# Performance work log

Measured on AMD Instinct MI355X. Metric: run time of the kernel, lower is better.

The kernel has to match this reference:

```python
import jax, jax.numpy as jnp
import numpy as np

L = 2048      # seq_len
E = 2048      # hidden_dim
H = 16        # num_heads
D = E // H    # head_dim


def setup_inputs() -> dict:
    key = jax.random.key(0)
    ks = jax.random.split(key, 6)
    x = jax.random.normal(ks[0], (L, E), dtype=jnp.float32)
    bias_matrix = jax.random.normal(ks[1], (L, L), dtype=jnp.float32) * 0.1
    # nn.MultiheadAttention params: packed in_proj [3E, E] + bias [3E], out_proj [E, E] + bias [E]
    in_proj_weight = jax.random.normal(ks[2], (3 * E, E), dtype=jnp.float32) * 0.02
    in_proj_bias = jax.random.normal(ks[3], (3 * E,), dtype=jnp.float32) * 0.02
    out_proj_weight = jax.random.normal(ks[4], (E, E), dtype=jnp.float32) * 0.02
    out_proj_bias = jax.random.normal(ks[5], (E,), dtype=jnp.float32) * 0.02
    return {
        "x": x,
        "bias_matrix": bias_matrix,
        "in_proj_weight": in_proj_weight,
        "in_proj_bias": in_proj_bias,
        "out_proj_weight": out_proj_weight,
        "out_proj_bias": out_proj_bias,
    }


def reference(x, bias_matrix, in_proj_weight, in_proj_bias, out_proj_weight, out_proj_bias):
    # Packed QKV projection (torch Linear convention: y = x @ W.T + b)
    qkv = x @ in_proj_weight.T + in_proj_bias            # [L, 3E]
    q, k, v = jnp.split(qkv, 3, axis=-1)                 # each [L, E]
    q = q.reshape(L, H, D)
    k = k.reshape(L, H, D)
    v = v.reshape(L, H, D)
    scale = 1.0 / jnp.sqrt(jnp.asarray(D, dtype=x.dtype))
    # scores: [H, L, L]; bias_matrix broadcast over heads (torch 2D attn_mask semantics)
    scores = jnp.einsum("lhd,mhd->hlm", q * scale, k) + bias_matrix[None, :, :]
    attn = jax.nn.softmax(scores, axis=-1)
    ctx = jnp.einsum("hlm,mhd->lhd", attn, v).reshape(L, E)
    out = ctx @ out_proj_weight.T + out_proj_bias        # [L, E]
    return out
```

## Files before the change

### kernel.cpp

```cpp
#include <hip/hip_runtime.h>
#include <math.h>

#define L_SEQ 2048
#define E_DIM 2048
#define H_NUM 16
#define D_HEAD 128

typedef __attribute__((ext_vector_type(8))) _Float16 half8;
typedef __attribute__((ext_vector_type(4))) _Float16 half4;
typedef __attribute__((ext_vector_type(4))) float floatx4;

static __device__ __forceinline__ void gload16(const void* g, void* lds) {
  __builtin_amdgcn_global_load_lds(
      (const __attribute__((address_space(1))) void*)g,
      (__attribute__((address_space(3))) void*)lds, 16, 0, 0);
}

__global__ __launch_bounds__(256)
void cvt3_f32_f16(const float* __restrict__ a, _Float16* __restrict__ oa, int na,
                  const float* __restrict__ b, _Float16* __restrict__ ob, int nb,
                  const float* __restrict__ c, _Float16* __restrict__ oc, int nc) {
  int i = (blockIdx.x * 256 + threadIdx.x) * 8;
  const float* src;
  _Float16* dst;
  if (i < na) {
    src = a + i; dst = oa + i;
  } else if (i < na + nb) {
    src = b + (i - na); dst = ob + (i - na);
  } else if (i < na + nb + nc) {
    src = c + (i - na - nb); dst = oc + (i - na - nb);
  } else {
    return;
  }
  float4 p = *(const float4*)src;
  float4 q = *(const float4*)(src + 4);
  half8 h = {(_Float16)p.x, (_Float16)p.y, (_Float16)p.z, (_Float16)p.w,
             (_Float16)q.x, (_Float16)q.y, (_Float16)q.z, (_Float16)q.w};
  *(half8*)dst = h;
}

__global__ __launch_bounds__(512, 1)
void gemm_qkv(const _Float16* __restrict__ A, const _Float16* __restrict__ B,
              const float* __restrict__ bias, _Float16* __restrict__ qk,
              _Float16* __restrict__ vt) {
  constexpr int K = E_DIM;
  __shared__ __align__(16) char smem[131072];
  char* const Asm = smem;
  char* const Bsm = smem + 32768;

  const int tid = threadIdx.x;
  const int wave = tid >> 6, lane = tid & 63;
  const int l15 = lane & 15, quad = lane >> 4;
  const int wm = wave >> 2, wn = wave & 3;

  const int lid = blockIdx.y * 16 + blockIdx.x;
  const int swz = (lid & 7) * 32 + (lid >> 3);
  const int brow = (swz >> 4) * 128, bcol = (swz & 15) * 384;

  const _Float16* Ag = A + (size_t)brow * K;
  const _Float16* Bg = B + (size_t)bcol * K;

  auto stg = [&](int T, int kh) {
    char* aslot = Asm + ((T & 1) * 2 + kh) * 8192;
    char* bslot = Bsm + ((T & 1) * 2 + kh) * 24576;
    {
      int row = tid >> 2, c = tid & 3;
      gload16(Ag + (size_t)row * K + T * 64 + kh * 32 +
                  ((c ^ ((row >> 1) & 3)) * 8),
              aslot + (tid & ~63) * 16);
    }
#pragma unroll
    for (int j = 0; j < 3; ++j) {
      int mb = j * 512 + (tid & ~63);
      int m = mb + (tid & 63);
      int row = m >> 2, c = m & 3;
      gload16(Bg + (size_t)row * K + T * 64 + kh * 32 +
                  ((c ^ ((row >> 1) & 3)) * 8),
              bslot + mb * 16);
    }
  };

  floatx4 acc[4][6];
#pragma unroll
  for (int i = 0; i < 4; ++i)
#pragma unroll
    for (int j = 0; j < 6; ++j) acc[i][j] = (floatx4){0.f, 0.f, 0.f, 0.f};

  auto compute_phase = [&](int T, int ks) {
    const char* Ab = Asm + ((T & 1) * 2 + ks) * 8192;
    const char* Bb = Bsm + ((T & 1) * 2 + ks) * 24576;
    half8 af[4], bf[6];
#pragma unroll
    for (int t = 0; t < 4; ++t) {
      int r = wm * 64 + t * 16 + l15;
      af[t] = *(const half8*)(Ab + (size_t)r * 64 +
                              ((quad ^ ((r >> 1) & 3)) * 16));
    }
#pragma unroll
    for (int t = 0; t < 6; ++t) {
      int r = wn * 96 + t * 16 + l15;
      bf[t] = *(const half8*)(Bb + (size_t)r * 64 +
                              ((quad ^ ((r >> 1) & 3)) * 16));
    }
#pragma unroll
    for (int i = 0; i < 4; ++i)
#pragma unroll
      for (int j = 0; j < 6; ++j)
        acc[i][j] = __builtin_amdgcn_mfma_f32_16x16x32_f16(af[i], bf[j],
                                                           acc[i][j], 0, 0, 0);
  };

  stg(0, 0); stg(0, 1); stg(1, 0);

  for (int T = 0; T < 31; ++T) {
    __builtin_amdgcn_sched_barrier(0);
    asm volatile("s_waitcnt vmcnt(8) lgkmcnt(0)" ::: "memory");
    __builtin_amdgcn_s_barrier();
    __builtin_amdgcn_sched_barrier(0);
    stg(T + 1, 1);
    compute_phase(T, 0);
    __builtin_amdgcn_sched_barrier(0);
    asm volatile("s_waitcnt vmcnt(8) lgkmcnt(0)" ::: "memory");
    __builtin_amdgcn_s_barrier();
    __builtin_amdgcn_sched_barrier(0);
    if (T < 30) stg(T + 2, 0);
    compute_phase(T, 1);
  }
  __builtin_amdgcn_sched_barrier(0);
  asm volatile("s_waitcnt vmcnt(4) lgkmcnt(0)" ::: "memory");
  __builtin_amdgcn_s_barrier();
  __builtin_amdgcn_sched_barrier(0);
  compute_phase(31, 0);
  __builtin_amdgcn_sched_barrier(0);
  asm volatile("s_waitcnt vmcnt(0) lgkmcnt(0)" ::: "memory");
  __builtin_amdgcn_s_barrier();
  __builtin_amdgcn_sched_barrier(0);
  compute_phase(31, 1);

  const int crow = brow + wm * 64;
  const int ccol0 = bcol + wn * 96;
#pragma unroll
  for (int j = 0; j < 6; ++j) {
    int col = ccol0 + j * 16 + l15;
    float bb = bias[col];
    if (col < 2 * E_DIM) {
#pragma unroll
      for (int i = 0; i < 4; ++i)
#pragma unroll
        for (int r = 0; r < 4; ++r)
          qk[(size_t)(crow + i * 16 + quad * 4 + r) * (2 * E_DIM) + col] =
              (_Float16)(acc[i][j][r] + bb);
    } else {
      int vrow = col - 2 * E_DIM;
#pragma unroll
      for (int i = 0; i < 4; ++i) {
        int rbase = crow + i * 16 + quad * 4;
        half4 h = {(_Float16)(acc[i][j][0] + bb), (_Float16)(acc[i][j][1] + bb),
                   (_Float16)(acc[i][j][2] + bb), (_Float16)(acc[i][j][3] + bb)};
        *(half4*)&vt[(size_t)vrow * L_SEQ + rbase] = h;
      }
    }
  }
}

template <int TM, int TN, int WR, int WC>
__global__ __launch_bounds__(256)
void gemm_mfma(const _Float16* __restrict__ A, const _Float16* __restrict__ B,
               const float* __restrict__ bias, float* __restrict__ C,
               int M, int N, int K) {
  constexpr int RT = TM / (16 * WR);
  constexpr int CT = TN / (16 * WC);
  constexpr int ACH = TM / 8;
  constexpr int NCH = (TM + TN) / 32;

  __shared__ _Float16 As[2][TM * 64];
  __shared__ _Float16 Bs[2][TN * 64];

  const int tid = threadIdx.x;
  const int wave = tid >> 6, lane = tid & 63;
  const int l15 = lane & 15, quad = lane >> 4;
  const int wr = wave / WC, wc = wave % WC;
  const int row0 = blockIdx.y * TM, col0 = blockIdx.x * TN;

  const int srow = lane >> 3;
  const int gc = (lane & 7) ^ srow;

  auto stage = [&](int buf, int k0) {
#pragma unroll
    for (int c = 0; c < NCH; ++c) {
      int chunk = wave * NCH + c;
      if (chunk < ACH) {
        int row = chunk * 8 + srow;
        gload16((const char*)(A + (size_t)(row0 + row) * K + k0) + gc * 16,
                (char*)&As[buf][0] + chunk * 1024);
      } else {
        int bch = chunk - ACH;
        int row = bch * 8 + srow;
        gload16((const char*)(B + (size_t)(col0 + row) * K + k0) + gc * 16,
                (char*)&Bs[buf][0] + bch * 1024);
      }
    }
  };

  floatx4 acc[RT][CT];
#pragma unroll
  for (int i = 0; i < RT; ++i)
#pragma unroll
    for (int j = 0; j < CT; ++j) acc[i][j] = (floatx4){0.f, 0.f, 0.f, 0.f};

  const int niter = K / 64;
  stage(0, 0);

  for (int it = 0; it < niter; ++it) {
    const int cur = it & 1;
    __syncthreads();
    if (it + 1 < niter) stage(cur ^ 1, (it + 1) * 64);

#pragma unroll
    for (int ks = 0; ks < 2; ++ks) {
      half8 af[RT], bf[CT];
#pragma unroll
      for (int t = 0; t < RT; ++t) {
        int r = wr * (16 * RT) + t * 16 + l15;
        af[t] = *(const half8*)&As[cur][r * 64 + (((ks * 4 + quad) ^ (r & 7)) * 8)];
      }
#pragma unroll
      for (int t = 0; t < CT; ++t) {
        int r = wc * (16 * CT) + t * 16 + l15;
        bf[t] = *(const half8*)&Bs[cur][r * 64 + (((ks * 4 + quad) ^ (r & 7)) * 8)];
      }
#pragma unroll
      for (int tr = 0; tr < RT; ++tr)
#pragma unroll
        for (int tc = 0; tc < CT; ++tc)
          acc[tr][tc] = __builtin_amdgcn_mfma_f32_16x16x32_f16(
              af[tr], bf[tc], acc[tr][tc], 0, 0, 0);
    }
  }

  const int crow = row0 + wr * (16 * RT);
  const int ccol = col0 + wc * (16 * CT);

#pragma unroll
  for (int tc = 0; tc < CT; ++tc) {
    int col = ccol + tc * 16 + l15;
    float bb = bias[col];
#pragma unroll
    for (int tr = 0; tr < RT; ++tr)
#pragma unroll
      for (int r = 0; r < 4; ++r)
        C[(size_t)(crow + tr * 16 + quad * 4 + r) * N + col] =
            acc[tr][tc][r] + bb;
  }
}

__global__ __launch_bounds__(512, 2)
void attn_mfma(const _Float16* __restrict__ qk, const _Float16* __restrict__ vt,
               const float* __restrict__ bias, _Float16* __restrict__ ctx) {
  const int h = blockIdx.x;
  const int q0 = blockIdx.y * 128;
  const int tid = threadIdx.x;
  const int wave = tid >> 6;
  const int lane = tid & 63;
  const int l15 = lane & 15;
  const int quad = lane >> 4;

  __shared__ _Float16 Ks[2][64][136];
  __shared__ _Float16 Vst[2][128][72];
  __shared__ _Float16 Ps[128][72];

  half8 qa[4];
  {
    const _Float16* qp = qk + (size_t)(q0 + wave * 16 + l15) * (2 * E_DIM) +
                         h * D_HEAD + quad * 8;
#pragma unroll
    for (int ks = 0; ks < 4; ++ks) qa[ks] = *(const half8*)(qp + ks * 32);
  }

  float l_i = 0.f;
  floatx4 o[8];
#pragma unroll
  for (int t = 0; t < 8; ++t) o[t] = (floatx4){0.f, 0.f, 0.f, 0.f};

  const float scale = 0.088388347648318447f;

  half8 kreg[2], vreg[2];
  floatx4 bcur[4], bnxt[4];
#pragma unroll
  for (int c = 0; c < 2; ++c) {
    int m = c * 512 + tid;
    kreg[c] = *(const half8*)(qk + (size_t)(m >> 4) * (2 * E_DIM) + E_DIM +
                              h * D_HEAD + (m & 15) * 8);
    vreg[c] = *(const half8*)(vt + (size_t)(h * D_HEAD + (m >> 3)) * L_SEQ +
                              (m & 7) * 8);
  }
#pragma unroll
  for (int t = 0; t < 4; ++t)
    bcur[t] = *(const floatx4*)&bias[(size_t)(q0 + wave * 16 + l15) * L_SEQ +
                                    16 * t + quad * 4];
#pragma unroll
  for (int c = 0; c < 2; ++c) {
    int m = c * 512 + tid;
    *(half8*)&Ks[0][m >> 4][(m & 15) * 8] = kreg[c];
    *(half8*)&Vst[0][m >> 3][(m & 7) * 8] = vreg[c];
  }

#pragma unroll 2
  for (int it = 0; it < 32; ++it) {
    const int cur = it & 1, nxt = cur ^ 1;
    const int kt = it * 64;
    __syncthreads();

    if (it < 31) {
#pragma unroll
      for (int c = 0; c < 2; ++c) {
        int m = c * 512 + tid;
        kreg[c] = *(const half8*)(qk + (size_t)(kt + 64 + (m >> 4)) * (2 * E_DIM) +
                                  E_DIM + h * D_HEAD + (m & 15) * 8);
        vreg[c] = *(const half8*)(vt + (size_t)(h * D_HEAD + (m >> 3)) * L_SEQ +
                                  kt + 64 + (m & 7) * 8);
      }
#pragma unroll
      for (int t = 0; t < 4; ++t)
        bnxt[t] = *(const floatx4*)&bias[(size_t)(q0 + wave * 16 + l15) * L_SEQ +
                                         kt + 64 + 16 * t + quad * 4];
    }

    floatx4 st[4];
#pragma unroll
    for (int t = 0; t < 4; ++t) st[t] = (floatx4){0.f, 0.f, 0.f, 0.f};
#pragma unroll
    for (int ks = 0; ks < 4; ++ks)
#pragma unroll
      for (int t = 0; t < 4; ++t) {
        half8 kf = *(const half8*)&Ks[cur][16 * t + l15][ks * 32 + quad * 8];
        st[t] = __builtin_amdgcn_mfma_f32_16x16x32_f16(kf, qa[ks], st[t], 0, 0, 0);
      }

    {
      float ls = 0.f;
      float ps[4][4];
#pragma unroll
      for (int t = 0; t < 4; ++t)
#pragma unroll
        for (int r = 0; r < 4; ++r) {
          float p = __expf(fmaf(st[t][r], scale, bcur[t][r]));
          ps[t][r] = p;
          ls += p;
        }
      ls += __shfl_xor(ls, 16);
      ls += __shfl_xor(ls, 32);
      l_i += ls;
#pragma unroll
      for (int t = 0; t < 4; ++t) {
        half4 hp = {(_Float16)ps[t][0], (_Float16)ps[t][1],
                    (_Float16)ps[t][2], (_Float16)ps[t][3]};
        *(half4*)&Ps[wave * 16 + l15][16 * t + quad * 4] = hp;
      }
    }

    half8 pa[2];
#pragma unroll
    for (int ks = 0; ks < 2; ++ks)
      pa[ks] = *(const half8*)&Ps[wave * 16 + l15][ks * 32 + quad * 8];
#pragma unroll
    for (int t = 0; t < 8; ++t)
#pragma unroll
      for (int ks = 0; ks < 2; ++ks) {
        half8 vf = *(const half8*)&Vst[cur][16 * t + l15][ks * 32 + quad * 8];
        o[t] = __builtin_amdgcn_mfma_f32_16x16x32_f16(pa[ks], vf, o[t], 0, 0, 0);
      }

    if (it < 31) {
#pragma unroll
      for (int c = 0; c < 2; ++c) {
        int m = c * 512 + tid;
        *(half8*)&Ks[nxt][m >> 4][(m & 15) * 8] = kreg[c];
        *(half8*)&Vst[nxt][m >> 3][(m & 7) * 8] = vreg[c];
      }
#pragma unroll
      for (int t = 0; t < 4; ++t) bcur[t] = bnxt[t];
    }
  }

  float inv[4];
#pragma unroll
  for (int r = 0; r < 4; ++r) inv[r] = 1.f / __shfl(l_i, quad * 4 + r);
#pragma unroll
  for (int t = 0; t < 8; ++t)
#pragma unroll
    for (int r = 0; r < 4; ++r) {
      int row = q0 + wave * 16 + quad * 4 + r;
      ctx[(size_t)row * E_DIM + h * D_HEAD + 16 * t + l15] =
          (_Float16)(o[t][r] * inv[r]);
    }
}

extern "C" void kernel_launch(void* const* d_in, const int* in_sizes, int n_in,
                              void* d_out, int out_size, void* d_ws, size_t ws_size,
                              hipStream_t stream) {
  const float* x          = (const float*)d_in[0];
  const float* bias_mat   = (const float*)d_in[1];
  const float* in_proj_w  = (const float*)d_in[2];
  const float* in_proj_b  = (const float*)d_in[3];
  const float* out_proj_w = (const float*)d_in[4];
  const float* out_proj_b = (const float*)d_in[5];
  float* out = (float*)d_out;

  _Float16* x16 = (_Float16*)d_ws;
  _Float16* w1  = x16 + (size_t)L_SEQ * E_DIM;
  _Float16* w2  = w1 + (size_t)3 * E_DIM * E_DIM;
  _Float16* qk  = w2 + (size_t)E_DIM * E_DIM;
  _Float16* vt  = qk + (size_t)L_SEQ * 2 * E_DIM;
  _Float16* ctx = vt + (size_t)E_DIM * L_SEQ;

  dim3 blk(256);
  const int nx = L_SEQ * E_DIM, nw1 = 3 * E_DIM * E_DIM, nw2 = E_DIM * E_DIM;

  cvt3_f32_f16<<<(nx + nw1 + nw2) / 2048, blk, 0, stream>>>(
      x, x16, nx, in_proj_w, w1, nw1, out_proj_w, w2, nw2);

  gemm_qkv<<<dim3(16, 16), dim3(512), 0, stream>>>(x16, w1, in_proj_b, qk, vt);

  attn_mfma<<<dim3(H_NUM, L_SEQ / 128), dim3(512), 0, stream>>>(qk, vt, bias_mat,
                                                                ctx);

  gemm_mfma<128, 64, 4, 1><<<dim3(E_DIM / 64, L_SEQ / 128), blk, 0, stream>>>(
      ctx, w2, out_proj_b, out, L_SEQ, E_DIM, E_DIM);
}
```

Baseline: 275.2 us.

## Replace out-projection GEMM with 128x128-tile pipelined kernel using half-K stages

Replaces the generic templated output-projection GEMM (128x64 tiles, 256 threads, double buffer) with a dedicated 512-thread kernel using 128x128 tiles. The K loop is split into 32-wide half stages with explicit vmcnt waits and sched barriers, so global-to-LDS loads overlap MFMA compute. The block index is also swizzled to improve L2 reuse. It cuts the number of blocks to 256 and relies on hand-tuned waitcnt values that must match the issue order of the loads.

New measurement: 283.9 us. +3.1%, slower.

```diff
diff --git a/kernel.cpp b/kernel.cpp
--- a/kernel.cpp
+++ b/kernel.cpp
@@ -163,94 +163,105 @@
   }
 }
 
-template <int TM, int TN, int WR, int WC>
-__global__ __launch_bounds__(256)
-void gemm_mfma(const _Float16* __restrict__ A, const _Float16* __restrict__ B,
-               const float* __restrict__ bias, float* __restrict__ C,
-               int M, int N, int K) {
-  constexpr int RT = TM / (16 * WR);
-  constexpr int CT = TN / (16 * WC);
-  constexpr int ACH = TM / 8;
-  constexpr int NCH = (TM + TN) / 32;
-
-  __shared__ _Float16 As[2][TM * 64];
-  __shared__ _Float16 Bs[2][TN * 64];
+__global__ __launch_bounds__(512, 2)
+void gemm_out(const _Float16* __restrict__ A, const _Float16* __restrict__ B,
+              const float* __restrict__ bias, float* __restrict__ C) {
+  constexpr int K = E_DIM;
+  constexpr int N = E_DIM;
+  __shared__ __align__(16) char smem[65536];
+  char* const Asm = smem;
+  char* const Bsm = smem + 32768;
 
   const int tid = threadIdx.x;
   const int wave = tid >> 6, lane = tid & 63;
   const int l15 = lane & 15, quad = lane >> 4;
-  const int wr = wave / WC, wc = wave % WC;
-  const int row0 = blockIdx.y * TM, col0 = blockIdx.x * TN;
-
-  const int srow = lane >> 3;
-  const int gc = (lane & 7) ^ srow;
-
-  auto stage = [&](int buf, int k0) {
-#pragma unroll
-    for (int c = 0; c < NCH; ++c) {
-      int chunk = wave * NCH + c;
-      if (chunk < ACH) {
-        int row = chunk * 8 + srow;
-        gload16((const char*)(A + (size_t)(row0 + row) * K + k0) + gc * 16,
-                (char*)&As[buf][0] + chunk * 1024);
-      } else {
-        int bch = chunk - ACH;
-        int row = bch * 8 + srow;
-        gload16((const char*)(B + (size_t)(col0 + row) * K + k0) + gc * 16,
-                (char*)&Bs[buf][0] + bch * 1024);
-      }
-    }
+  const int wm = wave >> 2, wn = wave & 3;
+
+  const int lid = blockIdx.y * 16 + blockIdx.x;
+  const int swz = (lid & 7) * 32 + (lid >> 3);
+  const int brow = (swz >> 4) * 128, bcol = (swz & 15) * 128;
+
+  const _Float16* Ag = A + (size_t)brow * K;
+  const _Float16* Bg = B + (size_t)bcol * K;
+
+  auto stg = [&](int T, int kh) {
+    char* aslot = Asm + ((T & 1) * 2 + kh) * 8192;
+    char* bslot = Bsm + ((T & 1) * 2 + kh) * 8192;
+    int row = tid >> 2, c = tid & 3;
+    int goff = T * 64 + kh * 32 + ((c ^ ((row >> 1) & 3)) * 8);
+    gload16(Ag + (size_t)row * K + goff, aslot + (tid & ~63) * 16);
+    gload16(Bg + (size_t)row * K + goff, bslot + (tid & ~63) * 16);
   };
 
-  floatx4 acc[RT][CT];
-#pragma unroll
-  for (int i = 0; i < RT; ++i)
-#pragma unroll
-    for (int j = 0; j < CT; ++j) acc[i][j] = (floatx4){0.f, 0.f, 0.f, 0.f};
-
-  const int niter = K / 64;
-  stage(0, 0);
-
-  for (int it = 0; it < niter; ++it) {
-    const int cur = it & 1;
-    __syncthreads();
-    if (it + 1 < niter) stage(cur ^ 1, (it + 1) * 64);
-
-#pragma unroll
-    for (int ks = 0; ks < 2; ++ks) {
-      half8 af[RT], bf[CT];
-#pragma unroll
-      for (int t = 0; t < RT; ++t) {
-        int r = wr * (16 * RT) + t * 16 + l15;
-        af[t] = *(const half8*)&As[cur][r * 64 + (((ks * 4 + quad) ^ (r & 7)) * 8)];
-      }
-#pragma unroll
-      for (int t = 0; t < CT; ++t) {
-        int r = wc * (16 * CT) + t * 16 + l15;
-        bf[t] = *(const half8*)&Bs[cur][r * 64 + (((ks * 4 + quad) ^ (r & 7)) * 8)];
-      }
-#pragma unroll
-      for (int tr = 0; tr < RT; ++tr)
-#pragma unroll
-        for (int tc = 0; tc < CT; ++tc)
-          acc[tr][tc] = __builtin_amdgcn_mfma_f32_16x16x32_f16(
-              af[tr], bf[tc], acc[tr][tc], 0, 0, 0);
-    }
-  }
-
-  const int crow = row0 + wr * (16 * RT);
-  const int ccol = col0 + wc * (16 * CT);
-
-#pragma unroll
-  for (int tc = 0; tc < CT; ++tc) {
-    int col = ccol + tc * 16 + l15;
+  floatx4 acc[4][2];
+#pragma unroll
+  for (int i = 0; i < 4; ++i)
+#pragma unroll
+    for (int j = 0; j < 2; ++j) acc[i][j] = (floatx4){0.f, 0.f, 0.f, 0.f};
+
+  auto compute_phase = [&](int T, int ks) {
+    const char* Ab = Asm + ((T & 1) * 2 + ks) * 8192;
+    const char* Bb = Bsm + ((T & 1) * 2 + ks) * 8192;
+    half8 af[4], bf[2];
+#pragma unroll
+    for (int t = 0; t < 4; ++t) {
+      int r = wm * 64 + t * 16 + l15;
+      af[t] = *(const half8*)(Ab + (size_t)r * 64 +
+                              ((quad ^ ((r >> 1) & 3)) * 16));
+    }
+#pragma unroll
+    for (int t = 0; t < 2; ++t) {
+      int r = wn * 32 + t * 16 + l15;
+      bf[t] = *(const half8*)(Bb + (size_t)r * 64 +
+                              ((quad ^ ((r >> 1) & 3)) * 16));
+    }
+#pragma unroll
+    for (int i = 0; i < 4; ++i)
+#pragma unroll
+      for (int j = 0; j < 2; ++j)
+        acc[i][j] = __builtin_amdgcn_mfma_f32_16x16x32_f16(af[i], bf[j],
+                                                           acc[i][j], 0, 0, 0);
+  };
+
+  stg(0, 0); stg(0, 1); stg(1, 0);
+
+  for (int T = 0; T < 31; ++T) {
+    __builtin_amdgcn_sched_barrier(0);
+    asm volatile("s_waitcnt vmcnt(4) lgkmcnt(0)" ::: "memory");
+    __builtin_amdgcn_s_barrier();
+    __builtin_amdgcn_sched_barrier(0);
+    stg(T + 1, 1);
+    compute_phase(T, 0);
+    __builtin_amdgcn_sched_barrier(0);
+    asm volatile("s_waitcnt vmcnt(4) lgkmcnt(0)" ::: "memory");
+    __builtin_amdgcn_s_barrier();
+    __builtin_amdgcn_sched_barrier(0);
+    if (T < 30) stg(T + 2, 0);
+    compute_phase(T, 1);
+  }
+  __builtin_amdgcn_sched_barrier(0);
+  asm volatile("s_waitcnt vmcnt(2) lgkmcnt(0)" ::: "memory");
+  __builtin_amdgcn_s_barrier();
+  __builtin_amdgcn_sched_barrier(0);
+  compute_phase(31, 0);
+  __builtin_amdgcn_sched_barrier(0);
+  asm volatile("s_waitcnt vmcnt(0) lgkmcnt(0)" ::: "memory");
+  __builtin_amdgcn_s_barrier();
+  __builtin_amdgcn_sched_barrier(0);
+  compute_phase(31, 1);
+
+  const int crow = brow + wm * 64;
+  const int ccol0 = bcol + wn * 32;
+#pragma unroll
+  for (int j = 0; j < 2; ++j) {
+    int col = ccol0 + j * 16 + l15;
     float bb = bias[col];
 #pragma unroll
-    for (int tr = 0; tr < RT; ++tr)
+    for (int i = 0; i < 4; ++i)
 #pragma unroll
       for (int r = 0; r < 4; ++r)
-        C[(size_t)(crow + tr * 16 + quad * 4 + r) * N + col] =
-            acc[tr][tc][r] + bb;
+        C[(size_t)(crow + i * 16 + quad * 4 + r) * N + col] =
+            acc[i][j][r] + bb;
   }
 }
 
@@ -425,6 +436,5 @@
   attn_mfma<<<dim3(H_NUM, L_SEQ / 128), dim3(512), 0, stream>>>(qk, vt, bias_mat,
                                                                 ctx);
 
-  gemm_mfma<128, 64, 4, 1><<<dim3(E_DIM / 64, L_SEQ / 128), blk, 0, stream>>>(
-      ctx, w2, out_proj_b, out, L_SEQ, E_DIM, E_DIM);
-}
+  gemm_out<<<dim3(16, 16), dim3(512), 0, stream>>>(ctx, w2, out_proj_b, out);
+}
```
